# Performance work log

Hardware: AMD Instinct MI355X
Metric: run time of the kernel (lower is better)

## Reference

```python
import jax, jax.numpy as jnp
import numpy as np

B, C, S, H, W = 1, 256, 64, 32, 128
BLOCKS, HEADS, DH = 2, 8, 32
SCALE = DH ** (-0.5)


def layer_norm(x, w, b, eps=1e-5):
    mu = jnp.mean(x, axis=-1, keepdims=True)
    var = jnp.var(x, axis=-1, keepdims=True)
    return (x - mu) * jax.lax.rsqrt(var + eps) * w + b


def generate_y_for_attn(y, u):
    # y: (B,C,H,W), u: (B,S,S) float -> (B, S^2, 2H, C)
    Bv, Cv, Hv, Wv = y.shape
    Sv = u.shape[1]
    uf = jnp.floor(u).reshape(Bv, Sv * Sv)
    u_left = jnp.clip(uf, 0, Wv - 1).astype(jnp.int32)
    u_right = jnp.clip(uf + 1, 0, Wv - 1).astype(jnp.int32)
    yf = y.reshape(Bv, Cv * Hv, Wv)

    def gather_w(idx):
        idxb = jnp.broadcast_to(idx[:, None, :], (Bv, Cv * Hv, Sv * Sv))
        return jnp.take_along_axis(yf, idxb, axis=2).reshape(Bv, Cv, Hv, Sv * Sv)

    ys = jnp.concatenate([gather_w(u_left), gather_w(u_right)], axis=2)  # (B,C,2H,S2)
    return ys.transpose(0, 3, 2, 1)  # (B, S2, 2H, C)


def cross_attention(x, y, p, i):
    # x: (B,M,C), y: (B,M,N,C)
    q = layer_norm(x, p['ln_q_w'][i], p['ln_q_b'][i]) @ p['Wq'][i]        # (B,M,HD)
    k = layer_norm(y, p['ln_k_w'][i], p['ln_k_b'][i]) @ p['Wk'][i]        # (B,M,N,HD)
    v = layer_norm(y, p['ln_v_w'][i], p['ln_v_b'][i]) @ p['Wv'][i]        # (B,M,N,HD)
    Bv, M, _ = q.shape
    N = k.shape[2]
    q = q.reshape(Bv, M, HEADS, DH)
    k = k.reshape(Bv, M, N, HEADS, DH)
    v = v.reshape(Bv, M, N, HEADS, DH)
    dot = SCALE * jnp.einsum('bmhd,bmnhd->bhmn', q, k)                    # (B,H,M,N)
    attn = jax.nn.softmax(dot, axis=-1)
    a = jnp.einsum('bhmn,bmnhd->bmhd', attn, v).reshape(Bv, M, HEADS * DH)
    z = a @ p['Wproj'][i] + p['bproj'][i]
    z = layer_norm(z, p['ln_pre_w'][i], p['ln_pre_b'][i])
    h = jax.nn.gelu(z @ p['Wm1'][i] + p['bm1'][i], approximate=False)
    z = z + (h @ p['Wm2'][i] + p['bm2'][i])
    return layer_norm(z, p['ln_post_w'][i], p['ln_post_b'][i])


def setup_inputs() -> dict:
    key = jax.random.key(0)
    ks = jax.random.split(key, 16)
    std = 0.02
    inp = {
        'grd2sat': jax.random.normal(ks[0], (B, C, S, S), jnp.float32),
        'grd_x': jax.random.normal(ks[1], (B, C, H, W), jnp.float32),
        'u': jax.random.uniform(ks[2], (B, S, S), jnp.float32) * (W - 1),
        'ln_q_w': jnp.ones((BLOCKS, C)), 'ln_q_b': jnp.zeros((BLOCKS, C)),
        'ln_k_w': jnp.ones((BLOCKS, C)), 'ln_k_b': jnp.zeros((BLOCKS, C)),
        'ln_v_w': jnp.ones((BLOCKS, C)), 'ln_v_b': jnp.zeros((BLOCKS, C)),
        'Wq': std * jax.random.normal(ks[3], (BLOCKS, C, HEADS * DH)),
        'Wk': std * jax.random.normal(ks[4], (BLOCKS, C, HEADS * DH)),
        'Wv': std * jax.random.normal(ks[5], (BLOCKS, C, HEADS * DH)),
        'Wproj': std * jax.random.normal(ks[6], (BLOCKS, HEADS * DH, C)),
        'bproj': jnp.zeros((BLOCKS, C)),
        'ln_pre_w': jnp.ones((BLOCKS, C)), 'ln_pre_b': jnp.zeros((BLOCKS, C)),
        'Wm1': std * jax.random.normal(ks[7], (BLOCKS, C, 2 * C)),
        'bm1': jnp.zeros((BLOCKS, 2 * C)),
        'Wm2': std * jax.random.normal(ks[8], (BLOCKS, 2 * C, C)),
        'bm2': jnp.zeros((BLOCKS, C)),
        'ln_post_w': jnp.ones((BLOCKS, C)), 'ln_post_b': jnp.zeros((BLOCKS, C)),
    }
    return inp


def reference(grd2sat, grd_x, u, ln_q_w, ln_q_b, ln_k_w, ln_k_b, ln_v_w, ln_v_b,
              Wq, Wk, Wv, Wproj, bproj, ln_pre_w, ln_pre_b, Wm1, bm1, Wm2, bm2,
              ln_post_w, ln_post_b):
    p = dict(ln_q_w=ln_q_w, ln_q_b=ln_q_b, ln_k_w=ln_k_w, ln_k_b=ln_k_b,
             ln_v_w=ln_v_w, ln_v_b=ln_v_b, Wq=Wq, Wk=Wk, Wv=Wv, Wproj=Wproj,
             bproj=bproj, ln_pre_w=ln_pre_w, ln_pre_b=ln_pre_b, Wm1=Wm1, bm1=bm1,
             Wm2=Wm2, bm2=bm2, ln_post_w=ln_post_w, ln_post_b=ln_post_b)
    y_attn = generate_y_for_attn(grd_x, u)               # (B, S^2, 2H, C)
    x = grd2sat.reshape(B, C, S * S).transpose(0, 2, 1)  # (B, M, C)
    for i in range(BLOCKS):
        # (Swin self-attention layer omitted; cross-attention stack only.)
        x = cross_attention(x, y_attn, p, i)
    out = x.transpose(0, 2, 1).reshape(B, C, S, S)
    # L2 normalize over channel dim
    norm = jnp.sqrt(jnp.sum(out * out, axis=1, keepdims=True))
    return out / jnp.maximum(norm, 1e-12)
```

## Files before the change

### kernel.cpp

```cpp
#include <hip/hip_runtime.h>
#include <math.h>


#define C_DIM 256
#define M_DIM 4096
#define ATT_SCALE 0.17677669529663687f

typedef __attribute__((ext_vector_type(8))) short short8;
typedef __attribute__((ext_vector_type(4))) short short4v;
typedef __attribute__((ext_vector_type(4))) float floatx4;

__device__ __forceinline__ unsigned short f2bf(float f) {
    unsigned u = __float_as_uint(f);
    unsigned r = (u + 0x7fffu + ((u >> 16) & 1u)) >> 16;
    return (unsigned short)r;
}
__device__ __forceinline__ float gelu_exact(float x) {
    return 0.5f * x * (1.0f + erff(x * 0.70710678118654752f));
}

struct PrepArgs {
    const float* grd2sat; float* xcur;
    const float* grd_x;   unsigned short* yhat;
    const float* u; int* perm; int4* chunks; int* nchunks;
    const float* win[12]; unsigned short* wout[12]; const float* wlnw[12];
    int wR[12], wC[12], wbase[13];
    const float* fW[10]; const float* flnb[10]; const float* fbase[10];
    float* fout[10];
    int fN[10], fwcol[10], focol[10];
};

__global__ __launch_bounds__(256) void prep_kernel(PrepArgs a) {
    __shared__ float smemf[9024];
    int b = blockIdx.x, t = threadIdx.x;
    if (b < 256) {
        float (*tile)[65] = (float(*)[65])smemf;
        int m0 = (b & 63) << 6, c0 = (b >> 6) << 6;
        for (int it = 0; it < 16; ++it) {
            int idx = it * 256 + t;
            int co = idx >> 6, mo = idx & 63;
            tile[co][mo] = a.grd2sat[(size_t)(c0 + co) * M_DIM + m0 + mo];
        }
        __syncthreads();
        for (int it = 0; it < 16; ++it) {
            int idx = it * 256 + t;
            int mo = idx >> 6, co = idx & 63;
            a.xcur[(size_t)(m0 + mo) * C_DIM + c0 + co] = tile[co][mo];
        }
    } else if (b < 384) {
        int idx = b - 256;
        int h = idx & 31, w0 = (idx >> 5) << 5;
        float (*tile)[33] = (float(*)[33])smemf;
        float (*ps)[32] = (float(*)[32])(smemf + 8448);
        float (*pss)[32] = (float(*)[32])(smemf + 8704);
        float* mu_s = smemf + 8960;
        float* rs_s = smemf + 8992;
        int wo = t & 31, cb = t >> 5;
        for (int it = 0; it < 32; ++it) {
            int c = it * 8 + cb;
            tile[c][wo] = a.grd_x[(size_t)c * 4096 + h * 128 + w0 + wo];
        }
        __syncthreads();
        {
            int w = t & 31, part = t >> 5;
            float s = 0.f, ss = 0.f;
            for (int c = part * 32; c < part * 32 + 32; ++c) {
                float x = tile[c][w];
                s += x; ss += x * x;
            }
            ps[part][w] = s; pss[part][w] = ss;
        }
        __syncthreads();
        if (t < 32) {
            float s = 0.f, ss = 0.f;
            for (int p = 0; p < 8; ++p) { s += ps[p][t]; ss += pss[p][t]; }
            float mu = s * (1.f / 256.f);
            float var = ss * (1.f / 256.f) - mu * mu;
            mu_s[t] = mu;
            rs_s[t] = rsqrtf(var + 1e-5f);
        }
        __syncthreads();
        for (int jj = 0; jj < 32; ++jj) {
            float mu = mu_s[jj], rs = rs_s[jj];
            a.yhat[((size_t)(w0 + jj) * 32 + h) * C_DIM + t] =
                f2bf((tile[t][jj] - mu) * rs);
        }
    } else if (b < 1408) {
        int wI = b - 384;
        int e = 0;
        while (wI >= a.wbase[e + 1]) ++e;
        int tl = wI - a.wbase[e];
        int tilesC = a.wC[e] >> 5;
        int tr = tl / tilesC, tc = tl - tr * tilesC;
        int r0 = tr << 5, c0 = tc << 5;
        const float* in = a.win[e];
        unsigned short* out = a.wout[e];
        const float* lnw = a.wlnw[e];
        int R = a.wR[e], Cc = a.wC[e];
        float (*tile)[33] = (float(*)[33])smemf;
        int rl = t >> 3, cq = (t & 7) << 2;
        float4 v = *(const float4*)&in[(size_t)(r0 + rl) * Cc + c0 + cq];
        if (lnw) {
            float s = lnw[r0 + rl];
            v.x *= s; v.y *= s; v.z *= s; v.w *= s;
        }
        tile[rl][cq + 0] = v.x;
        tile[rl][cq + 1] = v.y;
        tile[rl][cq + 2] = v.z;
        tile[rl][cq + 3] = v.w;
        __syncthreads();
        int cl = t >> 3, rq = (t & 7) << 2;
        ushort4 o;
        o.x = f2bf(tile[rq + 0][cl]);
        o.y = f2bf(tile[rq + 1][cl]);
        o.z = f2bf(tile[rq + 2][cl]);
        o.w = f2bf(tile[rq + 3][cl]);
        *(ushort4*)&out[(size_t)(c0 + cl) * R + r0 + rq] = o;
    } else if (b < 1448) {
        int idx = b - 1408;
        int jj = idx >> 2, part = idx & 3;
        int N = a.fN[jj];
        int c = t & 63, kp = t >> 6;
        int wcol = a.fwcol[jj] + (part << 6) + c;
        const float* W = a.fW[jj];
        const float* lb = a.flnb[jj];
        float s = 0.f;
#pragma unroll 4
        for (int k = kp * 64; k < kp * 64 + 64; ++k)
            s += lb[k] * W[(size_t)k * N + wcol];
        smemf[(kp << 6) + c] = s;
        __syncthreads();
        if (t < 64) {
            float tot = smemf[t] + smemf[64 + t] + smemf[128 + t] + smemf[192 + t];
            int ocol = a.focol[jj] + (part << 6) + t;
            if (a.fbase[jj]) tot += a.fbase[jj][a.fwcol[jj] + (part << 6) + t];
            a.fout[jj][ocol] = tot;
        }
    } else {
        int* hist = (int*)smemf;
        int* cur = (int*)smemf + 128;
        unsigned short* wlb = (unsigned short*)((int*)smemf + 256);
        if (t < 128) hist[t] = 0;
        __syncthreads();
        for (int it = 0; it < 16; ++it) {
            int m = it * 256 + t;
            int wl = (int)floorf(a.u[m]);
            wl = max(0, min(wl, 126));
            wlb[m] = (unsigned short)wl;
            atomicAdd(&hist[wl], 1);
        }
        __syncthreads();
        if (t == 0) {
            int run = 0, nc = 0;
            for (int bkt = 0; bkt < 127; ++bkt) {
                int c = hist[bkt];
                cur[bkt] = run;
                int q0 = run;
                while (c > 0) {
                    int take = min(c, 32);
                    a.chunks[nc] = make_int4(bkt, q0, take, 0);
                    ++nc; q0 += take; c -= take;
                }
                run += hist[bkt];
            }
            *a.nchunks = nc;
        }
        __syncthreads();
        for (int it = 0; it < 16; ++it) {
            int m = it * 256 + t;
            int wl = wlb[m];
            int pos = atomicAdd(&cur[wl], 1);
            a.perm[pos] = m;
        }
    }
}

struct GJ {
    const void* A; const unsigned short* Bt;
    const float* bias;
    void* out; unsigned short* out2;
    int K, N;
};

__device__ __forceinline__ void gemm_core_kv(const GJ& j, short (*As)[264],
                                             short (*Bs)[264], int bm, int by) {
    int t = threadIdx.x;
    int bn = by << 6;
    int wv = t >> 6, lane = t & 63;
    int mt = wv & 1, nt0 = (wv >> 1) << 1;
    int quad = lane >> 4, l16 = lane & 15;
    floatx4 acc0 = {0.f, 0.f, 0.f, 0.f};
    floatx4 acc1 = {0.f, 0.f, 0.f, 0.f};
    {
        int ar = t >> 3, cq = (t & 7) << 5;
        const unsigned short* ap =
            (const unsigned short*)j.A + (size_t)(bm + ar) * 256 + cq;
#pragma unroll
        for (int c = 0; c < 4; ++c)
            *(uint4*)&As[ar][cq + (c << 3)] = *(const uint4*)(ap + (c << 3));
    }
    {
        int br = t >> 2, cq2 = (t & 3) << 3;
        const unsigned short* bp = j.Bt + (size_t)(bn + br) * 256 + cq2;
#pragma unroll
        for (int g = 0; g < 8; ++g)
            *(short8*)&Bs[br][cq2 + g * 32] = *(const short8*)(bp + g * 32);
    }
    __syncthreads();
#pragma unroll
    for (int k0 = 0; k0 < 8; ++k0) {
        short8 aa = *(const short8*)&As[(mt << 4) + l16][(k0 << 5) + (quad << 3)];
        short8 b0 = *(const short8*)&Bs[(nt0 << 4) + l16][(k0 << 5) + (quad << 3)];
        short8 b1 =
            *(const short8*)&Bs[((nt0 + 1) << 4) + l16][(k0 << 5) + (quad << 3)];
        acc0 = __builtin_amdgcn_mfma_f32_16x16x32_bf16(aa, b0, acc0, 0, 0, 0);
        acc1 = __builtin_amdgcn_mfma_f32_16x16x32_bf16(aa, b1, acc1, 0, 0, 0);
    }
#pragma unroll
    for (int jj = 0; jj < 2; ++jj) {
        const floatx4 accv = jj ? acc1 : acc0;
        int col = bn + ((nt0 + jj) << 4) + l16;
        float bv = j.bias[col];
#pragma unroll
        for (int r = 0; r < 4; ++r) {
            int row = bm + (mt << 4) + (quad << 2) + r;
            float v = accv[r] + bv;
            if (col < 256)
                ((unsigned short*)j.out)[(size_t)row * 256 + col] = f2bf(v);
            else
                j.out2[(size_t)(col - 256) * M_DIM + row] = f2bf(v);
        }
    }
}

__global__ __launch_bounds__(256) void kv_kernel(GJ j0, GJ j1) {
    __shared__ short As[32][264];
    __shared__ short Bs[64][264];
    int bm = blockIdx.x << 5;
    if ((int)blockIdx.y < 8)
        gemm_core_kv(j0, As, Bs, bm, blockIdx.y);
    else
        gemm_core_kv(j1, As, Bs, bm, blockIdx.y - 8);
}

struct MegaArgs {
    const float* xcur;
    const int* perm; const int4* chunks; const int* nchunks;
    float* xfinal;
    const unsigned short* Wq[2]; const unsigned short* Wp[2];
    const unsigned short* Wm1[2]; const unsigned short* Wm2[2];
    const unsigned short* Ktb[2]; const unsigned short* Vtb[2];
    const float* qb[2]; const float* m1b[2];
    const float* bpj[2]; const float* bm2v[2];
    const float* pw[2]; const float* pb[2];
    const float* aw; const float* ab;
};

struct BPre { short8 b[8][2]; };

__device__ __forceinline__ void preloadB(const unsigned short* Bt, int Kstride,
                                         int koff, int colw, int l16, int quad,
                                         BPre& P) {
    const unsigned short* bp =
        Bt + (size_t)(colw + l16) * Kstride + koff + (quad << 3);
#pragma unroll
    for (int k0 = 0; k0 < 8; ++k0)
#pragma unroll
        for (int ni = 0; ni < 2; ++ni)
            P.b[k0][ni] =
                *(const short8*)(bp + (size_t)(ni << 4) * Kstride + (k0 << 5));
}

__device__ __forceinline__ void mfma32t(const short* As, int lda, const BPre& P,
                                        int l16, int quad, floatx4 acc[2][2]) {
    const short* ap = As + (size_t)l16 * lda + (quad << 3);
#pragma unroll
    for (int k0 = 0; k0 < 8; ++k0) {
        short8 a0 = *(const short8*)(ap + (k0 << 5));
        short8 a1 = *(const short8*)(ap + (size_t)16 * lda + (k0 << 5));
        acc[0][0] = __builtin_amdgcn_mfma_f32_16x16x32_bf16(a0, P.b[k0][0], acc[0][0], 0, 0, 0);
        acc[0][1] = __builtin_amdgcn_mfma_f32_16x16x32_bf16(a0, P.b[k0][1], acc[0][1], 0, 0, 0);
        acc[1][0] = __builtin_amdgcn_mfma_f32_16x16x32_bf16(a1, P.b[k0][0], acc[1][0], 0, 0, 0);
        acc[1][1] = __builtin_amdgcn_mfma_f32_16x16x32_bf16(a1, P.b[k0][1], acc[1][1], 0, 0, 0);
    }
}

#define ZACC(A) \
    { A[0][0] = (floatx4){0.f,0.f,0.f,0.f}; A[0][1] = (floatx4){0.f,0.f,0.f,0.f}; \
      A[1][0] = (floatx4){0.f,0.f,0.f,0.f}; A[1][1] = (floatx4){0.f,0.f,0.f,0.f}; }

__global__ __launch_bounds__(512) void mega_kernel(MegaArgs a) {
    __shared__ __align__(16) char smem[137856];
    short (*XH)[264] = (short(*)[264])(smem);
    short (*QR)[264] = (short(*)[264])(smem + 16896);
    short (*ZH)[264] = (short(*)[264])(smem + 33792);
    short (*AR)[264] = (short(*)[264])(smem + 50688);
    float (*Zf)[260] = (float(*)[260])(smem + 67584);
    short (*PB)[32][72] = (short(*)[32][72])(smem + 100864);
    int* gp = (int*)(smem + 137728);

    if ((int)blockIdx.x >= *a.nchunks) return;
    int4 cd = a.chunks[blockIdx.x];
    int wl = cd.x, qstart = cd.y, qcnt = cd.z;
    int t = threadIdx.x;
    if (t < 32) gp[t] = (t < qcnt) ? a.perm[qstart + t] : a.perm[qstart];
    __syncthreads();

    int wv = t >> 6, lane = t & 63, quad = lane >> 4, l16 = lane & 15;
    int colw = wv << 5;
    int r16 = t >> 4, c0 = (t & 15) << 4;

    BPre Pq;
    preloadB(a.Wq[0], 256, 0, colw, l16, quad, Pq);

#pragma unroll 1
    for (int l = 0; l < 2; ++l) {
        {
            float4 v[4];
            if (l == 0) {
                const float* xp = a.xcur + (size_t)gp[r16] * 256 + c0;
#pragma unroll
                for (int g4 = 0; g4 < 4; ++g4)
                    v[g4] = *(const float4*)(xp + (g4 << 2));
            } else {
#pragma unroll
                for (int g4 = 0; g4 < 4; ++g4)
                    v[g4] = *(const float4*)&Zf[r16][c0 + (g4 << 2)];
            }
            float s = 0.f, ss = 0.f;
#pragma unroll
            for (int g4 = 0; g4 < 4; ++g4) {
                s += v[g4].x + v[g4].y + v[g4].z + v[g4].w;
                ss += v[g4].x * v[g4].x + v[g4].y * v[g4].y + v[g4].z * v[g4].z +
                      v[g4].w * v[g4].w;
            }
#pragma unroll
            for (int o = 1; o < 16; o <<= 1) {
                s += __shfl_xor(s, o, 64);
                ss += __shfl_xor(ss, o, 64);
            }
            float mu = s * (1.f / 256.f);
            float rs = rsqrtf(ss * (1.f / 256.f) - mu * mu + 1e-5f);
#pragma unroll
            for (int g4 = 0; g4 < 4; ++g4) {
                v[g4].x = (v[g4].x - mu) * rs;
                v[g4].y = (v[g4].y - mu) * rs;
                v[g4].z = (v[g4].z - mu) * rs;
                v[g4].w = (v[g4].w - mu) * rs;
            }
            if (l == 1) {
                float s2 = 0.f, ss2 = 0.f;
#pragma unroll
                for (int g4 = 0; g4 < 4; ++g4) {
                    float4 w4 = *(const float4*)&a.aw[c0 + (g4 << 2)];
                    float4 b4 = *(const float4*)&a.ab[c0 + (g4 << 2)];
                    v[g4].x = v[g4].x * w4.x + b4.x;
                    v[g4].y = v[g4].y * w4.y + b4.y;
                    v[g4].z = v[g4].z * w4.z + b4.z;
                    v[g4].w = v[g4].w * w4.w + b4.w;
                    s2 += v[g4].x + v[g4].y + v[g4].z + v[g4].w;
                    ss2 += v[g4].x * v[g4].x + v[g4].y * v[g4].y +
                           v[g4].z * v[g4].z + v[g4].w * v[g4].w;
                }
#pragma unroll
                for (int o = 1; o < 16; o <<= 1) {
                    s2 += __shfl_xor(s2, o, 64);
                    ss2 += __shfl_xor(ss2, o, 64);
                }
                float mu2 = s2 * (1.f / 256.f);
                float rs2 = rsqrtf(ss2 * (1.f / 256.f) - mu2 * mu2 + 1e-5f);
#pragma unroll
                for (int g4 = 0; g4 < 4; ++g4) {
                    v[g4].x = (v[g4].x - mu2) * rs2;
                    v[g4].y = (v[g4].y - mu2) * rs2;
                    v[g4].z = (v[g4].z - mu2) * rs2;
                    v[g4].w = (v[g4].w - mu2) * rs2;
                }
            }
#pragma unroll
            for (int g4 = 0; g4 < 4; ++g4) {
                short4v o;
                o[0] = (short)f2bf(v[g4].x);
                o[1] = (short)f2bf(v[g4].y);
                o[2] = (short)f2bf(v[g4].z);
                o[3] = (short)f2bf(v[g4].w);
                *(short4v*)&XH[r16][c0 + (g4 << 2)] = o;
            }
        }
        __syncthreads();

        short8 kb[4], vfrag[2][2];
        {
            const unsigned short* Kt = a.Ktb[l];
            const unsigned short* Vt = a.Vtb[l];
            int h = wv;
#pragma unroll
            for (int nt = 0; nt < 4; ++nt)
                kb[nt] = *(const short8*)(
                    Kt + (size_t)((wl << 5) + (nt << 4) + l16) * 256 +
                    (h << 5) + (quad << 3));
#pragma unroll
            for (int ks = 0; ks < 2; ++ks)
#pragma unroll
                for (int dt = 0; dt < 2; ++dt)
                    vfrag[ks][dt] = *(const short8*)(
                        Vt + (size_t)((h << 5) + (dt << 4) + l16) * M_DIM +
                        (wl << 5) + (ks << 5) + (quad << 3));
        }
        {
            floatx4 acc[2][2];
            ZACC(acc);
            mfma32t((const short*)XH, 264, Pq, l16, quad, acc);
            const float* qb = a.qb[l];
#pragma unroll
            for (int ni = 0; ni < 2; ++ni) {
                int col = colw + (ni << 4) + l16;
                float bv = qb[col];
#pragma unroll
                for (int mi = 0; mi < 2; ++mi)
#pragma unroll
                    for (int r = 0; r < 4; ++r)
                        QR[(mi << 4) + (quad << 2) + r][col] =
                            (short)f2bf(acc[mi][ni][r] + bv);
            }
        }
        __syncthreads();

        BPre Pp;
        preloadB(a.Wp[l], 256, 0, colw, l16, quad, Pp);
        {
            int h = wv;
            short8 aq0 = *(const short8*)&QR[l16][(h << 5) + (quad << 3)];
            short8 aq1 = *(const short8*)&QR[16 + l16][(h << 5) + (quad << 3)];
            floatx4 c[2][4];
#pragma unroll
            for (int nt = 0; nt < 4; ++nt) {
                floatx4 z = {0.f, 0.f, 0.f, 0.f};
                c[0][nt] = __builtin_amdgcn_mfma_f32_16x16x32_bf16(aq0, kb[nt], z, 0, 0, 0);
                c[1][nt] = __builtin_amdgcn_mfma_f32_16x16x32_bf16(aq1, kb[nt], z, 0, 0, 0);
            }
            floatx4 ri[2];
#pragma unroll
            for (int m = 0; m < 2; ++m) {
#pragma unroll
                for (int nt = 0; nt < 4; ++nt) {
                    floatx4 e;
#pragma unroll
                    for (int r = 0; r < 4; ++r)
                        e[r] = __expf(c[m][nt][r] * ATT_SCALE);
                    c[m][nt] = e;
                }
                floatx4 s4 = c[m][0] + c[m][1] + c[m][2] + c[m][3];
#pragma unroll
                for (int r = 0; r < 4; ++r) {
                    float s = s4[r];
                    s += __shfl_xor(s, 1, 64);
                    s += __shfl_xor(s, 2, 64);
                    s += __shfl_xor(s, 4, 64);
                    s += __shfl_xor(s, 8, 64);
                    ri[m][r] = 1.f / s;
                }
            }
#pragma unroll
            for (int m = 0; m < 2; ++m)
#pragma unroll
                for (int nt = 0; nt < 4; ++nt)
#pragma unroll
                    for (int r = 0; r < 4; ++r)
                        PB[wv][(m << 4) + (quad << 2) + r][(nt << 4) + l16] =
                            (short)f2bf(c[m][nt][r] * ri[m][r]);
            __threadfence_block();
            floatx4 o[2][2];
#pragma unroll
            for (int m = 0; m < 2; ++m)
#pragma unroll
                for (int dt = 0; dt < 2; ++dt)
                    o[m][dt] = (floatx4){0.f, 0.f, 0.f, 0.f};
#pragma unroll
            for (int ks = 0; ks < 2; ++ks) {
                short8 pa0 =
                    *(const short8*)&PB[wv][l16][(ks << 5) + (quad << 3)];
                short8 pa1 =
                    *(const short8*)&PB[wv][16 + l16][(ks << 5) + (quad << 3)];
#pragma unroll
                for (int dt = 0; dt < 2; ++dt) {
                    o[0][dt] = __builtin_amdgcn_mfma_f32_16x16x32_bf16(
                        pa0, vfrag[ks][dt], o[0][dt], 0, 0, 0);
                    o[1][dt] = __builtin_amdgcn_mfma_f32_16x16x32_bf16(
                        pa1, vfrag[ks][dt], o[1][dt], 0, 0, 0);
                }
            }
            int h5 = wv << 5;
#pragma unroll
            for (int m = 0; m < 2; ++m)
#pragma unroll
                for (int dt = 0; dt < 2; ++dt)
#pragma unroll
                    for (int r = 0; r < 4; ++r)
                        AR[(m << 4) + (quad << 2) + r]
                          [h5 + (dt << 4) + l16] = (short)f2bf(o[m][dt][r]);
        }
        __syncthreads();

        BPre Pm1a;
        preloadB(a.Wm1[l], 256, 0, colw, l16, quad, Pm1a);
        {
            floatx4 acc[2][2];
            ZACC(acc);
            mfma32t((const short*)AR, 264, Pp, l16, quad, acc);
            const float* bpj = a.bpj[l];
#pragma unroll
            for (int ni = 0; ni < 2; ++ni) {
                int col = colw + (ni << 4) + l16;
                float bv = bpj[col];
#pragma unroll
                for (int mi = 0; mi < 2; ++mi)
#pragma unroll
                    for (int r = 0; r < 4; ++r)
                        Zf[(mi << 4) + (quad << 2) + r][col] = acc[mi][ni][r] + bv;
            }
        }
        __syncthreads();

        {
            const float* pw = a.pw[l];
            const float* pb = a.pb[l];
            float4 v[4];
#pragma unroll
            for (int g4 = 0; g4 < 4; ++g4)
                v[g4] = *(const float4*)&Zf[r16][c0 + (g4 << 2)];
            float s = 0.f, ss = 0.f;
#pragma unroll
            for (int g4 = 0; g4 < 4; ++g4) {
                s += v[g4].x + v[g4].y + v[g4].z + v[g4].w;
                ss += v[g4].x * v[g4].x + v[g4].y * v[g4].y + v[g4].z * v[g4].z +
                      v[g4].w * v[g4].w;
            }
#pragma unroll
            for (int o = 1; o < 16; o <<= 1) {
                s += __shfl_xor(s, o, 64);
                ss += __shfl_xor(ss, o, 64);
            }
            float mu = s * (1.f / 256.f);
            float rs = rsqrtf(ss * (1.f / 256.f) - mu * mu + 1e-5f);
#pragma unroll
            for (int g4 = 0; g4 < 4; ++g4) {
                float4 z;
                z.x = (v[g4].x - mu) * rs;
                z.y = (v[g4].y - mu) * rs;
                z.z = (v[g4].z - mu) * rs;
                z.w = (v[g4].w - mu) * rs;
                short4v o;
                o[0] = (short)f2bf(z.x);
                o[1] = (short)f2bf(z.y);
                o[2] = (short)f2bf(z.z);
                o[3] = (short)f2bf(z.w);
                *(short4v*)&ZH[r16][c0 + (g4 << 2)] = o;
                float4 w4 = *(const float4*)&pw[c0 + (g4 << 2)];
                float4 b4 = *(const float4*)&pb[c0 + (g4 << 2)];
                float4 za;
                za.x = z.x * w4.x + b4.x;
                za.y = z.y * w4.y + b4.y;
                za.z = z.z * w4.z + b4.z;
                za.w = z.w * w4.w + b4.w;
                *(float4*)&Zf[r16][c0 + (g4 << 2)] = za;
            }
        }
        __syncthreads();

        const float* m1b = a.m1b[l];
        BPre Pm2a;
        {
            BPre Pm1b;
            preloadB(a.Wm1[l] + (size_t)256 * 256, 256, 0, colw, l16, quad,
                     Pm1b);
            floatx4 acc[2][2];
            ZACC(acc);
            mfma32t((const short*)ZH, 264, Pm1a, l16, quad, acc);
#pragma unroll
            for (int ni = 0; ni < 2; ++ni) {
                int col = colw + (ni << 4) + l16;
                float bv = m1b[col];
#pragma unroll
                for (int mi = 0; mi < 2; ++mi)
#pragma unroll
                    for (int r = 0; r < 4; ++r)
                        XH[(mi << 4) + (quad << 2) + r][col] =
                            (short)f2bf(gelu_exact(acc[mi][ni][r] + bv));
            }
            preloadB(a.Wm2[l], 512, 0, colw, l16, quad, Pm2a);
            floatx4 acc2[2][2];
            ZACC(acc2);
            mfma32t((const short*)ZH, 264, Pm1b, l16, quad, acc2);
#pragma unroll
            for (int ni = 0; ni < 2; ++ni) {
                int col = colw + (ni << 4) + l16;
                float bv = m1b[256 + col];
#pragma unroll
                for (int mi = 0; mi < 2; ++mi)
#pragma unroll
                    for (int r = 0; r < 4; ++r)
                        QR[(mi << 4) + (quad << 2) + r][col] =
                            (short)f2bf(gelu_exact(acc2[mi][ni][r] + bv));
            }
        }
        __syncthreads();

        {
            BPre Pm2b;
            preloadB(a.Wm2[l], 512, 256, colw, l16, quad, Pm2b);
            floatx4 macc[2][2];
            ZACC(macc);
            mfma32t((const short*)XH, 264, Pm2a, l16, quad, macc);
            mfma32t((const short*)QR, 264, Pm2b, l16, quad, macc);
            const float* b2 = a.bm2v[l];
#pragma unroll
            for (int ni = 0; ni < 2; ++ni) {
                int col = colw + (ni << 4) + l16;
                float bv = b2[col];
#pragma unroll
                for (int mi = 0; mi < 2; ++mi)
#pragma unroll
                    for (int r = 0; r < 4; ++r) {
                        int row = (mi << 4) + (quad << 2) + r;
                        float v = macc[mi][ni][r] + bv + Zf[row][col];
                        if (l == 0) {
                            Zf[row][col] = v;
                        } else if (row < qcnt) {
                            a.xfinal[(size_t)gp[row] * 256 + col] = v;
                        }
                    }
            }
            if (l == 0)
                preloadB(a.Wq[1], 256, 0, colw, l16, quad, Pq);
        }
        __syncthreads();
    }
}

__global__ __launch_bounds__(256) void out_kernel(const float* __restrict__ X,
                                                  const float* __restrict__ w,
                                                  const float* __restrict__ b,
                                                  float* __restrict__ out) {
    __shared__ float tile[32][261];
    int t = threadIdx.x;
    int mo = t >> 3, q = t & 7;
    int m0 = blockIdx.x << 5;
    const float* p = X + (size_t)(m0 + mo) * C_DIM + (q << 5);
    float4 v[8];
    float s = 0.f, ss = 0.f;
#pragma unroll
    for (int c = 0; c < 8; ++c) {
        v[c] = *(const float4*)(p + c * 4);
        s += v[c].x + v[c].y + v[c].z + v[c].w;
        ss += v[c].x * v[c].x + v[c].y * v[c].y + v[c].z * v[c].z + v[c].w * v[c].w;
    }
    s += __shfl_xor(s, 1, 64); s += __shfl_xor(s, 2, 64); s += __shfl_xor(s, 4, 64);
    ss += __shfl_xor(ss, 1, 64); ss += __shfl_xor(ss, 2, 64); ss += __shfl_xor(ss, 4, 64);
    float mu = s * (1.f / 256.f);
    float rs = rsqrtf(ss * (1.f / 256.f) - mu * mu + 1e-5f);
    float ss2 = 0.f;
#pragma unroll
    for (int c = 0; c < 8; ++c) {
        float4 w4 = *(const float4*)&w[(q << 5) + c * 4];
        float4 b4 = *(const float4*)&b[(q << 5) + c * 4];
        v[c].x = (v[c].x - mu) * rs * w4.x + b4.x;
        v[c].y = (v[c].y - mu) * rs * w4.y + b4.y;
        v[c].z = (v[c].z - mu) * rs * w4.z + b4.z;
        v[c].w = (v[c].w - mu) * rs * w4.w + b4.w;
        ss2 += v[c].x * v[c].x + v[c].y * v[c].y + v[c].z * v[c].z + v[c].w * v[c].w;
    }
    ss2 += __shfl_xor(ss2, 1, 64); ss2 += __shfl_xor(ss2, 2, 64); ss2 += __shfl_xor(ss2, 4, 64);
    float sc = 1.f / fmaxf(sqrtf(ss2), 1e-12f);
#pragma unroll
    for (int c = 0; c < 8; ++c) {
        tile[mo][(q << 5) + c * 4 + 0] = v[c].x * sc;
        tile[mo][(q << 5) + c * 4 + 1] = v[c].y * sc;
        tile[mo][(q << 5) + c * 4 + 2] = v[c].z * sc;
        tile[mo][(q << 5) + c * 4 + 3] = v[c].w * sc;
    }
    __syncthreads();
#pragma unroll 1
    for (int it = 0; it < 32; ++it) {
        int idx = it * 256 + t;
        int c = idx >> 5, m = idx & 31;
        out[(size_t)c * M_DIM + m0 + m] = tile[m][c];
    }
}

extern "C" void kernel_launch(void* const* d_in, const int* in_sizes, int n_in,
                              void* d_out, int out_size, void* d_ws, size_t ws_size,
                              hipStream_t stream) {
    const float* grd2sat = (const float*)d_in[0];
    const float* grd_x   = (const float*)d_in[1];
    const float* u       = (const float*)d_in[2];
    const float* ln_q_w  = (const float*)d_in[3];
    const float* ln_q_b  = (const float*)d_in[4];
    const float* ln_k_w  = (const float*)d_in[5];
    const float* ln_k_b  = (const float*)d_in[6];
    const float* ln_v_w  = (const float*)d_in[7];
    const float* ln_v_b  = (const float*)d_in[8];
    const float* Wq      = (const float*)d_in[9];
    const float* Wk      = (const float*)d_in[10];
    const float* Wv      = (const float*)d_in[11];
    const float* Wproj   = (const float*)d_in[12];
    const float* bproj   = (const float*)d_in[13];
    const float* ln_pre_w = (const float*)d_in[14];
    const float* ln_pre_b = (const float*)d_in[15];
    const float* Wm1     = (const float*)d_in[16];
    const float* bm1     = (const float*)d_in[17];
    const float* Wm2     = (const float*)d_in[18];
    const float* bm2     = (const float*)d_in[19];
    const float* ln_post_w = (const float*)d_in[20];
    const float* ln_post_b = (const float*)d_in[21];

    float* ws   = (float*)d_ws;
    unsigned short* yhat = (unsigned short*)ws;
    float* xcur = ws + 1048576;
    float* zq   = ws + 2097152;
    unsigned short* Ktab0 = (unsigned short*)(ws + 6291456);
    unsigned short* Vt0   = (unsigned short*)(ws + 6815744);
    unsigned short* Ktab1 = (unsigned short*)(ws + 7340032);
    unsigned short* Vt1   = (unsigned short*)(ws + 7864320);
    unsigned short* Bt    = (unsigned short*)(ws + 8388608);
    float* biasbuf = ws + 8912896;
    int*  perm    = (int*)(ws + 8915456);
    int4* chunks  = (int4*)(ws + 8919552);
    int*  nchunks = (int*)(ws + 8921600);
    const size_t BS = 524288;
    const size_t OQ = 0, OKV = 65536, OP = 196608, OM1 = 262144, OM2 = 393216;

    dim3 b256(256);

    PrepArgs pa;
    pa.grd2sat = grd2sat; pa.xcur = xcur;
    pa.grd_x = grd_x;     pa.yhat = yhat;
    pa.u = u; pa.perm = perm; pa.chunks = chunks; pa.nchunks = nchunks;
    {
        int base = 0;
        for (int i = 0; i < 2; ++i) {
            int e = 6 * i;
            unsigned short* bt = Bt + i * BS;
            pa.win[e+0] = Wq + i * 65536;    pa.wout[e+0] = bt + OQ;
            pa.wlnw[e+0] = ln_q_w + i * 256; pa.wR[e+0] = 256; pa.wC[e+0] = 256;
            pa.win[e+1] = Wk + i * 65536;    pa.wout[e+1] = bt + OKV;
            pa.wlnw[e+1] = ln_k_w + i * 256; pa.wR[e+1] = 256; pa.wC[e+1] = 256;
            pa.win[e+2] = Wv + i * 65536;    pa.wout[e+2] = bt + OKV + 65536;
            pa.wlnw[e+2] = ln_v_w + i * 256; pa.wR[e+2] = 256; pa.wC[e+2] = 256;
            pa.win[e+3] = Wproj + i * 65536; pa.wout[e+3] = bt + OP;
            pa.wlnw[e+3] = nullptr;          pa.wR[e+3] = 256; pa.wC[e+3] = 256;
            pa.win[e+4] = Wm1 + i * 131072;  pa.wout[e+4] = bt + OM1;
            pa.wlnw[e+4] = ln_pre_w + i * 256; pa.wR[e+4] = 256; pa.wC[e+4] = 512;
            pa.win[e+5] = Wm2 + i * 131072;  pa.wout[e+5] = bt + OM2;
            pa.wlnw[e+5] = nullptr;          pa.wR[e+5] = 512; pa.wC[e+5] = 256;
        }
        for (int e = 0; e < 12; ++e) {
            pa.wbase[e] = base;
            base += (pa.wR[e] >> 5) * (pa.wC[e] >> 5);
        }
        pa.wbase[12] = base;
        for (int i = 0; i < 2; ++i) {
            int jb = 5 * i;
            float* bb = biasbuf + i * 1280;
            pa.fW[jb+0] = Wq + i * 65536; pa.flnb[jb+0] = ln_q_b + i * 256;
            pa.fbase[jb+0] = nullptr; pa.fout[jb+0] = bb;
            pa.fN[jb+0] = 256; pa.fwcol[jb+0] = 0; pa.focol[jb+0] = 0;
            pa.fW[jb+1] = Wk + i * 65536; pa.flnb[jb+1] = ln_k_b + i * 256;
            pa.fbase[jb+1] = nullptr; pa.fout[jb+1] = bb + 256;
            pa.fN[jb+1] = 256; pa.fwcol[jb+1] = 0; pa.focol[jb+1] = 0;
            pa.fW[jb+2] = Wv + i * 65536; pa.flnb[jb+2] = ln_v_b + i * 256;
            pa.fbase[jb+2] = nullptr; pa.fout[jb+2] = bb + 256;
            pa.fN[jb+2] = 256; pa.fwcol[jb+2] = 0; pa.focol[jb+2] = 256;
            pa.fW[jb+3] = Wm1 + i * 131072; pa.flnb[jb+3] = ln_pre_b + i * 256;
            pa.fbase[jb+3] = bm1 + i * 512; pa.fout[jb+3] = bb + 768;
            pa.fN[jb+3] = 512; pa.fwcol[jb+3] = 0; pa.focol[jb+3] = 0;
            pa.fW[jb+4] = Wm1 + i * 131072; pa.flnb[jb+4] = ln_pre_b + i * 256;
            pa.fbase[jb+4] = bm1 + i * 512; pa.fout[jb+4] = bb + 768;
            pa.fN[jb+4] = 512; pa.fwcol[jb+4] = 256; pa.focol[jb+4] = 256;
        }
    }
    prep_kernel<<<1449, b256, 0, stream>>>(pa);

    GJ jkv0 = {};
    jkv0.A = yhat; jkv0.Bt = Bt + OKV; jkv0.bias = biasbuf + 256;
    jkv0.out = Ktab0; jkv0.out2 = Vt0; jkv0.K = 256; jkv0.N = 512;
    GJ jkv1 = {};
    jkv1.A = yhat; jkv1.Bt = Bt + BS + OKV; jkv1.bias = biasbuf + 1280 + 256;
    jkv1.out = Ktab1; jkv1.out2 = Vt1; jkv1.K = 256; jkv1.N = 512;
    kv_kernel<<<dim3(128, 16), b256, 0, stream>>>(jkv0, jkv1);

    MegaArgs ma;
    ma.xcur = xcur; ma.perm = perm; ma.chunks = chunks; ma.nchunks = nchunks;
    ma.xfinal = zq;
    for (int i = 0; i < 2; ++i) {
        const unsigned short* bt = Bt + i * BS;
        ma.Wq[i] = bt + OQ; ma.Wp[i] = bt + OP;
        ma.Wm1[i] = bt + OM1; ma.Wm2[i] = bt + OM2;
        ma.Ktb[i] = i ? Ktab1 : Ktab0; ma.Vtb[i] = i ? Vt1 : Vt0;
        ma.qb[i] = biasbuf + i * 1280;
        ma.m1b[i] = biasbuf + i * 1280 + 768;
        ma.bpj[i] = bproj + i * 256;
        ma.bm2v[i] = bm2 + i * 256;
        ma.pw[i] = ln_pre_w + i * 256;
        ma.pb[i] = ln_pre_b + i * 256;
    }
    ma.aw = ln_post_w; ma.ab = ln_post_b;
    mega_kernel<<<288, dim3(512), 0, stream>>>(ma);

    out_kernel<<<128, b256, 0, stream>>>(zq, ln_post_w + 256, ln_post_b + 256,
                                         (float*)d_out);
}
```

Before: 211.8 us.

## Fuse final layernorm and L2 normalize into mega kernel, reorder weight preloads

Drops the separate out_kernel and the fp32 intermediate buffer. The mega kernel now applies the last post-layernorm and the channel L2 normalization from shared memory and writes the transposed output directly. Weight-fragment preloads are moved later, next to their uses, to shorten register live ranges, and one __syncthreads after the Q projection becomes a block fence. The direct transposed stores are strided by M_DIM and uncoalesced, and relaxing the barrier relies on each wave reading only its own head's Q columns.

```diff
diff --git a/kernel.cpp b/kernel.cpp
--- a/kernel.cpp
+++ b/kernel.cpp
@@ -246,7 +246,6 @@
 struct MegaArgs {
     const float* xcur;
     const int* perm; const int4* chunks; const int* nchunks;
-    float* xfinal;
     const unsigned short* Wq[2]; const unsigned short* Wp[2];
     const unsigned short* Wm1[2]; const unsigned short* Wm2[2];
     const unsigned short* Ktb[2]; const unsigned short* Vtb[2];
@@ -254,6 +253,8 @@
     const float* bpj[2]; const float* bm2v[2];
     const float* pw[2]; const float* pb[2];
     const float* aw; const float* ab;
+    const float* ow; const float* ob;
+    float* oout;
 };
 
 struct BPre { short8 b[8][2]; };
@@ -310,11 +311,10 @@
     int colw = wv << 5;
     int r16 = t >> 4, c0 = (t & 15) << 4;
 
-    BPre Pq;
-    preloadB(a.Wq[0], 256, 0, colw, l16, quad, Pq);
-
 #pragma unroll 1
     for (int l = 0; l < 2; ++l) {
+        BPre Pq;
+        preloadB(a.Wq[l], 256, 0, colw, l16, quad, Pq);
         {
             float4 v[4];
             if (l == 0) {
@@ -424,10 +424,9 @@
                             (short)f2bf(acc[mi][ni][r] + bv);
             }
         }
-        __syncthreads();
+        __threadfence_block();
 
         BPre Pp;
-        preloadB(a.Wp[l], 256, 0, colw, l16, quad, Pp);
         {
             int h = wv;
             short8 aq0 = *(const short8*)&QR[l16][(h << 5) + (quad << 3)];
@@ -470,6 +469,7 @@
                         PB[wv][(m << 4) + (quad << 2) + r][(nt << 4) + l16] =
                             (short)f2bf(c[m][nt][r] * ri[m][r]);
             __threadfence_block();
+            preloadB(a.Wp[l], 256, 0, colw, l16, quad, Pp);
             floatx4 o[2][2];
 #pragma unroll
             for (int m = 0; m < 2; ++m)
@@ -502,8 +502,6 @@
         }
         __syncthreads();
 
-        BPre Pm1a;
-        preloadB(a.Wm1[l], 256, 0, colw, l16, quad, Pm1a);
         {
             floatx4 acc[2][2];
             ZACC(acc);
@@ -522,6 +520,8 @@
         }
         __syncthreads();
 
+        BPre Pm1a;
+        preloadB(a.Wm1[l], 256, 0, colw, l16, quad, Pm1a);
         {
             const float* pw = a.pw[l];
             const float* pb = a.pb[l];
@@ -571,12 +571,11 @@
         const float* m1b = a.m1b[l];
         BPre Pm2a;
         {
-            BPre Pm1b;
-            preloadB(a.Wm1[l] + (size_t)256 * 256, 256, 0, colw, l16, quad,
-                     Pm1b);
             floatx4 acc[2][2];
             ZACC(acc);
             mfma32t((const short*)ZH, 264, Pm1a, l16, quad, acc);
+            BPre Pm1b;
+            preloadB(a.Wm1[l] + (size_t)256 * 256, 256, 0, colw, l16, quad, Pm1b);
 #pragma unroll
             for (int ni = 0; ni < 2; ++ni) {
                 int col = colw + (ni << 4) + l16;
@@ -588,10 +587,10 @@
                         XH[(mi << 4) + (quad << 2) + r][col] =
                             (short)f2bf(gelu_exact(acc[mi][ni][r] + bv));
             }
-            preloadB(a.Wm2[l], 512, 0, colw, l16, quad, Pm2a);
             floatx4 acc2[2][2];
             ZACC(acc2);
             mfma32t((const short*)ZH, 264, Pm1b, l16, quad, acc2);
+            preloadB(a.Wm2[l], 512, 0, colw, l16, quad, Pm2a);
 #pragma unroll
             for (int ni = 0; ni < 2; ++ni) {
                 int col = colw + (ni << 4) + l16;
@@ -607,11 +606,11 @@
         __syncthreads();
 
         {
-            BPre Pm2b;
-            preloadB(a.Wm2[l], 512, 256, colw, l16, quad, Pm2b);
             floatx4 macc[2][2];
             ZACC(macc);
             mfma32t((const short*)XH, 264, Pm2a, l16, quad, macc);
+            BPre Pm2b;
+            preloadB(a.Wm2[l], 512, 256, colw, l16, quad, Pm2b);
             mfma32t((const short*)QR, 264, Pm2b, l16, quad, macc);
             const float* b2 = a.bm2v[l];
 #pragma unroll
@@ -623,68 +622,59 @@
 #pragma unroll
                     for (int r = 0; r < 4; ++r) {
                         int row = (mi << 4) + (quad << 2) + r;
-                        float v = macc[mi][ni][r] + bv + Zf[row][col];
-                        if (l == 0) {
-                            Zf[row][col] = v;
-                        } else if (row < qcnt) {
-                            a.xfinal[(size_t)gp[row] * 256 + col] = v;
-                        }
+                        Zf[row][col] = macc[mi][ni][r] + bv + Zf[row][col];
                     }
             }
-            if (l == 0)
-                preloadB(a.Wq[1], 256, 0, colw, l16, quad, Pq);
-        }
-        __syncthreads();
-    }
-}
-
-__global__ __launch_bounds__(256) void out_kernel(const float* __restrict__ X,
-                                                  const float* __restrict__ w,
-                                                  const float* __restrict__ b,
-                                                  float* __restrict__ out) {
-    __shared__ float tile[32][261];
-    int t = threadIdx.x;
-    int mo = t >> 3, q = t & 7;
-    int m0 = blockIdx.x << 5;
-    const float* p = X + (size_t)(m0 + mo) * C_DIM + (q << 5);
-    float4 v[8];
-    float s = 0.f, ss = 0.f;
-#pragma unroll
-    for (int c = 0; c < 8; ++c) {
-        v[c] = *(const float4*)(p + c * 4);
-        s += v[c].x + v[c].y + v[c].z + v[c].w;
-        ss += v[c].x * v[c].x + v[c].y * v[c].y + v[c].z * v[c].z + v[c].w * v[c].w;
-    }
-    s += __shfl_xor(s, 1, 64); s += __shfl_xor(s, 2, 64); s += __shfl_xor(s, 4, 64);
-    ss += __shfl_xor(ss, 1, 64); ss += __shfl_xor(ss, 2, 64); ss += __shfl_xor(ss, 4, 64);
-    float mu = s * (1.f / 256.f);
-    float rs = rsqrtf(ss * (1.f / 256.f) - mu * mu + 1e-5f);
-    float ss2 = 0.f;
-#pragma unroll
-    for (int c = 0; c < 8; ++c) {
-        float4 w4 = *(const float4*)&w[(q << 5) + c * 4];
-        float4 b4 = *(const float4*)&b[(q << 5) + c * 4];
-        v[c].x = (v[c].x - mu) * rs * w4.x + b4.x;
-        v[c].y = (v[c].y - mu) * rs * w4.y + b4.y;
-        v[c].z = (v[c].z - mu) * rs * w4.z + b4.z;
-        v[c].w = (v[c].w - mu) * rs * w4.w + b4.w;
-        ss2 += v[c].x * v[c].x + v[c].y * v[c].y + v[c].z * v[c].z + v[c].w * v[c].w;
-    }
-    ss2 += __shfl_xor(ss2, 1, 64); ss2 += __shfl_xor(ss2, 2, 64); ss2 += __shfl_xor(ss2, 4, 64);
-    float sc = 1.f / fmaxf(sqrtf(ss2), 1e-12f);
-#pragma unroll
-    for (int c = 0; c < 8; ++c) {
-        tile[mo][(q << 5) + c * 4 + 0] = v[c].x * sc;
-        tile[mo][(q << 5) + c * 4 + 1] = v[c].y * sc;
-        tile[mo][(q << 5) + c * 4 + 2] = v[c].z * sc;
-        tile[mo][(q << 5) + c * 4 + 3] = v[c].w * sc;
-    }
-    __syncthreads();
-#pragma unroll 1
-    for (int it = 0; it < 32; ++it) {
-        int idx = it * 256 + t;
-        int c = idx >> 5, m = idx & 31;
-        out[(size_t)c * M_DIM + m0 + m] = tile[m][c];
+        }
+        __syncthreads();
+    }
+
+    {
+        float4 v[4];
+#pragma unroll
+        for (int g4 = 0; g4 < 4; ++g4)
+            v[g4] = *(const float4*)&Zf[r16][c0 + (g4 << 2)];
+        float s = 0.f, ss = 0.f;
+#pragma unroll
+        for (int g4 = 0; g4 < 4; ++g4) {
+            s += v[g4].x + v[g4].y + v[g4].z + v[g4].w;
+            ss += v[g4].x * v[g4].x + v[g4].y * v[g4].y + v[g4].z * v[g4].z +
+                  v[g4].w * v[g4].w;
+        }
+#pragma unroll
+        for (int o = 1; o < 16; o <<= 1) {
+            s += __shfl_xor(s, o, 64);
+            ss += __shfl_xor(ss, o, 64);
+        }
+        float mu = s * (1.f / 256.f);
+        float rs = rsqrtf(ss * (1.f / 256.f) - mu * mu + 1e-5f);
+        float ss2 = 0.f;
+#pragma unroll
+        for (int g4 = 0; g4 < 4; ++g4) {
+            float4 w4 = *(const float4*)&a.ow[c0 + (g4 << 2)];
+            float4 b4 = *(const float4*)&a.ob[c0 + (g4 << 2)];
+            v[g4].x = (v[g4].x - mu) * rs * w4.x + b4.x;
+            v[g4].y = (v[g4].y - mu) * rs * w4.y + b4.y;
+            v[g4].z = (v[g4].z - mu) * rs * w4.z + b4.z;
+            v[g4].w = (v[g4].w - mu) * rs * w4.w + b4.w;
+            ss2 += v[g4].x * v[g4].x + v[g4].y * v[g4].y + v[g4].z * v[g4].z +
+                   v[g4].w * v[g4].w;
+        }
+#pragma unroll
+        for (int o = 1; o < 16; o <<= 1) ss2 += __shfl_xor(ss2, o, 64);
+        float sc = 1.f / fmaxf(sqrtf(ss2), 1e-12f);
+        if (r16 < qcnt) {
+            int m = gp[r16];
+            float* op = a.oout + m;
+#pragma unroll
+            for (int g4 = 0; g4 < 4; ++g4) {
+                int cb = c0 + (g4 << 2);
+                op[(size_t)(cb + 0) * M_DIM] = v[g4].x * sc;
+                op[(size_t)(cb + 1) * M_DIM] = v[g4].y * sc;
+                op[(size_t)(cb + 2) * M_DIM] = v[g4].z * sc;
+                op[(size_t)(cb + 3) * M_DIM] = v[g4].w * sc;
+            }
+        }
     }
 }
 
@@ -717,7 +707,6 @@
     float* ws   = (float*)d_ws;
     unsigned short* yhat = (unsigned short*)ws;
     float* xcur = ws + 1048576;
-    float* zq   = ws + 2097152;
     unsigned short* Ktab0 = (unsigned short*)(ws + 6291456);
     unsigned short* Vt0   = (unsigned short*)(ws + 6815744);
     unsigned short* Ktab1 = (unsigned short*)(ws + 7340032);
@@ -791,7 +780,6 @@
 
     MegaArgs ma;
     ma.xcur = xcur; ma.perm = perm; ma.chunks = chunks; ma.nchunks = nchunks;
-    ma.xfinal = zq;
     for (int i = 0; i < 2; ++i) {
         const unsigned short* bt = Bt + i * BS;
         ma.Wq[i] = bt + OQ; ma.Wp[i] = bt + OP;
@@ -805,8 +793,7 @@
         ma.pb[i] = ln_pre_b + i * 256;
     }
     ma.aw = ln_post_w; ma.ab = ln_post_b;
+    ma.ow = ln_post_w + 256; ma.ob = ln_post_b + 256;
+    ma.oout = (float*)d_out;
     mega_kernel<<<288, dim3(512), 0, stream>>>(ma);
-
-    out_kernel<<<128, b256, 0, stream>>>(zq, ln_post_w + 256, ln_post_b + 256,
-                                         (float*)d_out);
-}
+}
```

New measurement: 204.5 us. 1.04x faster.
